# Kernel tuning notes

Hardware: AMD Instinct MI355X
Metric: run time of the kernel (lower is better)

## Reference

```python
import jax, jax.numpy as jnp
import numpy as np

EMBED = 2048
HEADS = 32
HEAD_DIM = EMBED // HEADS
ALPHA = 12.0
MAX_SEQ = 1024
GAMMA = -ALPHA / MAX_SEQ  # clipped softmax lower stretch
ETA = 1.0


def setup_inputs() -> dict:
    key = jax.random.key(0)
    ks = jax.random.split(key, 12)
    B, T, E, H, D = 4, 1024, EMBED, HEADS, HEAD_DIM
    s = 1.0 / np.sqrt(E)
    hidden_states = jax.random.normal(ks[0], (B, T, E), dtype=jnp.float32)
    # causal attention mask: True = attend
    causal = jnp.tril(jnp.ones((T, T), dtype=bool))
    attention_mask = jnp.broadcast_to(causal[None, None], (B, 1, T, T))
    Wq = jax.random.normal(ks[1], (E, E), dtype=jnp.float32) * s
    bq = jnp.zeros((E,), dtype=jnp.float32)
    Wk = jax.random.normal(ks[2], (E, E), dtype=jnp.float32) * s
    bk = jnp.zeros((E,), dtype=jnp.float32)
    Wv = jax.random.normal(ks[3], (E, E), dtype=jnp.float32) * s
    bv = jnp.zeros((E,), dtype=jnp.float32)
    Wo = jax.random.normal(ks[4], (E, E), dtype=jnp.float32) * s
    bo = jnp.zeros((E,), dtype=jnp.float32)
    gate_w = jax.random.normal(ks[5], (H, D), dtype=jnp.float32) * (1.0 / np.sqrt(D))
    gate_b = jnp.zeros((H,), dtype=jnp.float32)
    return {"hidden_states": hidden_states, "attention_mask": attention_mask,
            "Wq": Wq, "bq": bq, "Wk": Wk, "bk": bk, "Wv": Wv, "bv": bv,
            "Wo": Wo, "bo": bo, "gate_w": gate_w, "gate_b": gate_b}


def clipped_softmax(x, gamma, eta):
    p = jax.nn.softmax(x, axis=-1)
    return jnp.clip((eta - gamma) * p + gamma, 0.0, 1.0)


def reference(hidden_states, attention_mask, Wq, bq, Wk, bk, Wv, bv, Wo, bo, gate_w, gate_b):
    B, T, E = hidden_states.shape
    H, D = HEADS, HEAD_DIM
    scaling = D ** -0.5
    neg_min = jnp.finfo(hidden_states.dtype).min

    q = ((hidden_states @ Wq.T + bq) * scaling).reshape(B, T, H, D)
    k = (hidden_states @ Wk.T + bk).reshape(B, T, H, D)
    v = (hidden_states @ Wv.T + bv).reshape(B, T, H, D)

    # scores: [B,H,T,S]
    scores = jnp.einsum('bthd,bshd->bhts', q, k)
    mask_add = jnp.where(attention_mask, 0.0, neg_min)  # [B,1,T,S]
    scores = jnp.maximum(scores + mask_add, neg_min)

    probs = clipped_softmax(scores, GAMMA, ETA)

    attn_out = jnp.einsum('bhts,bshd->bhtd', probs, v)  # [B,H,T,D]

    # conditional_per_token gate: per-head Linear(head_dim -> 1), sigmoid
    x_heads = hidden_states.reshape(B, T, H, D)
    gate = jax.nn.sigmoid(jnp.einsum('bthd,hd->bht', x_heads, gate_w) + gate_b[None, :, None])
    attn_out = attn_out * gate[..., None]  # gate_scaling_factor = 1.0

    out = attn_out.transpose(0, 2, 1, 3).reshape(B, T, E)
    return out @ Wo.T + bo
```

## Files before the change

### kernel.cpp

```cpp
#include <hip/hip_runtime.h>
#include <hip/hip_bf16.h>

typedef unsigned short ushort_t;
using short8 = __attribute__((ext_vector_type(8))) short;
using f32x4  = __attribute__((ext_vector_type(4))) float;

constexpr int B_ = 4;
constexpr int T_ = 1024;
constexpr int E_ = 2048;
constexpr int H_ = 32;
constexpr int D_ = 64;
constexpr float GAMMA_  = -12.0f / 1024.0f;
constexpr float ONE_MG_ = 1.0f - GAMMA_;

__device__ __forceinline__ ushort_t f2bf(float f) {
  union { float f; unsigned int i; } x; x.f = f;
  unsigned int u = x.i;
  u += 0x7fffu + ((u >> 16) & 1u);
  return (ushort_t)(u >> 16);
}

__global__ __launch_bounds__(256) void f2bf_multi(
    const float* __restrict__ x,
    const float* __restrict__ Wq, const float* __restrict__ Wk,
    const float* __restrict__ Wv, const float* __restrict__ Wo,
    ushort_t* __restrict__ xb,
    ushort_t* __restrict__ wqb, ushort_t* __restrict__ wkb,
    ushort_t* __restrict__ wvb, ushort_t* __restrict__ wob) {
  const int i = blockIdx.x * 256 + threadIdx.x;
  const float* src; ushort_t* dst; int off;
  if (i < 2097152)      { src = x;  dst = xb;  off = i; }
  else if (i < 3145728) { src = Wq; dst = wqb; off = i - 2097152; }
  else if (i < 4194304) { src = Wk; dst = wkb; off = i - 3145728; }
  else if (i < 5242880) { src = Wv; dst = wvb; off = i - 4194304; }
  else                  { src = Wo; dst = wob; off = i - 5242880; }
  const float4 f = ((const float4*)src)[off];
  ushort4 u; u.x = f2bf(f.x); u.y = f2bf(f.y); u.z = f2bf(f.z); u.w = f2bf(f.w);
  ((ushort4*)dst)[off] = u;
}

__device__ __forceinline__ void gl_lds16(const ushort_t* g, ushort_t* l) {
  __builtin_amdgcn_global_load_lds(
      (const __attribute__((address_space(1))) void*)g,
      (__attribute__((address_space(3))) void*)l, 16, 0, 0);
}

__global__ __launch_bounds__(256) void gemm_qkv(
    const ushort_t* __restrict__ xb,
    const ushort_t* __restrict__ wq, const ushort_t* __restrict__ wk,
    const ushort_t* __restrict__ wv,
    const float* __restrict__ bq, const float* __restrict__ bk,
    const float* __restrict__ bv,
    ushort_t* __restrict__ qout, ushort_t* __restrict__ kout,
    ushort_t* __restrict__ vtout) {
  constexpr int K = 2048;
  __shared__ ushort_t As[128 * 32];
  __shared__ ushort_t Bs[128 * 32];
  const int which = blockIdx.x >> 4;
  const int colt  = blockIdx.x & 15;
  const ushort_t* Wt  = (which == 0) ? wq : (which == 1) ? wk : wv;
  const float*   bias = (which == 0) ? bq : (which == 1) ? bk : bv;
  const float    scale = (which == 0) ? 0.125f : 1.0f;

  const int tid = threadIdx.x;
  const int wave = tid >> 6, lane = tid & 63;
  const int lane15 = lane & 15, quad = lane >> 4;
  const int row0 = blockIdx.y * 128, col0 = colt * 128;
  const int srow = lane >> 2;
  const int scol = (lane & 3) * 8;
  const ushort_t* Ag0 = xb + (size_t)(row0 + wave * 32 + srow) * K + scol;
  const ushort_t* Ag1 = Ag0 + 16 * (size_t)K;
  const ushort_t* Bg0 = Wt + (size_t)(col0 + wave * 32 + srow) * K + scol;
  const ushort_t* Bg1 = Bg0 + 16 * (size_t)K;
  ushort_t* Al0 = &As[(wave * 32     ) * 32];
  ushort_t* Al1 = &As[(wave * 32 + 16) * 32];
  ushort_t* Bl0 = &Bs[(wave * 32     ) * 32];
  ushort_t* Bl1 = &Bs[(wave * 32 + 16) * 32];
  const int wr = wave >> 1, wc = wave & 1;
  const int q8 = quad * 8;

  f32x4 acc[4][4];
#pragma unroll
  for (int i = 0; i < 4; i++)
#pragma unroll
    for (int j = 0; j < 4; j++) acc[i][j] = (f32x4){0.f, 0.f, 0.f, 0.f};

  for (int k0 = 0; k0 < K; k0 += 32) {
    __syncthreads();
    gl_lds16(Ag0 + k0, Al0);
    gl_lds16(Ag1 + k0, Al1);
    gl_lds16(Bg0 + k0, Bl0);
    gl_lds16(Bg1 + k0, Bl1);
    __syncthreads();
    short8 a_f[4], b_f[4];
#pragma unroll
    for (int i = 0; i < 4; i++)
      a_f[i] = *(const short8*)&As[(wr * 64 + i * 16 + lane15) * 32 + q8];
#pragma unroll
    for (int j = 0; j < 4; j++)
      b_f[j] = *(const short8*)&Bs[(wc * 64 + j * 16 + lane15) * 32 + q8];
#pragma unroll
    for (int i = 0; i < 4; i++)
#pragma unroll
      for (int j = 0; j < 4; j++)
        acc[i][j] = __builtin_amdgcn_mfma_f32_16x16x32_bf16(
            a_f[i], b_f[j], acc[i][j], 0, 0, 0);
  }

  ushort_t* outp = (which == 0) ? qout : (which == 1) ? kout : vtout;
#pragma unroll
  for (int j = 0; j < 4; j++) {
    const int c = col0 + wc * 64 + j * 16 + lane15;
    const float bia = bias[c];
#pragma unroll
    for (int i = 0; i < 4; i++) {
#pragma unroll
      for (int reg = 0; reg < 4; reg++) {
        const int r = row0 + wr * 64 + i * 16 + quad * 4 + reg;
        const float val = (acc[i][j][reg] + bia) * scale;
        const int b = r >> 10, t = r & 1023, h = c >> 6, d = c & 63;
        if (which < 2)
          outp[(((size_t)(b * 32 + h)) * 1024 + t) * 64 + d] = f2bf(val);
        else
          outp[(((size_t)(b * 32 + h)) * 64 + d) * 1024 + t] = f2bf(val);
      }
    }
  }
}

__global__ __launch_bounds__(256) void gemm_out(
    const ushort_t* __restrict__ A, const ushort_t* __restrict__ Wt,
    const float* __restrict__ bias, float* __restrict__ Cout) {
  constexpr int K = 2048;
  __shared__ ushort_t As[128 * 32];
  __shared__ ushort_t Bs[128 * 32];
  const int tid = threadIdx.x;
  const int wave = tid >> 6, lane = tid & 63;
  const int lane15 = lane & 15, quad = lane >> 4;
  const int row0 = blockIdx.y * 128, col0 = blockIdx.x * 128;
  const int srow = lane >> 2;
  const int scol = (lane & 3) * 8;
  const ushort_t* Ag0 = A  + (size_t)(row0 + wave * 32 + srow) * K + scol;
  const ushort_t* Ag1 = Ag0 + 16 * (size_t)K;
  const ushort_t* Bg0 = Wt + (size_t)(col0 + wave * 32 + srow) * K + scol;
  const ushort_t* Bg1 = Bg0 + 16 * (size_t)K;
  ushort_t* Al0 = &As[(wave * 32     ) * 32];
  ushort_t* Al1 = &As[(wave * 32 + 16) * 32];
  ushort_t* Bl0 = &Bs[(wave * 32     ) * 32];
  ushort_t* Bl1 = &Bs[(wave * 32 + 16) * 32];
  const int wr = wave >> 1, wc = wave & 1;
  const int q8 = quad * 8;

  f32x4 acc[4][4];
#pragma unroll
  for (int i = 0; i < 4; i++)
#pragma unroll
    for (int j = 0; j < 4; j++) acc[i][j] = (f32x4){0.f, 0.f, 0.f, 0.f};

  for (int k0 = 0; k0 < K; k0 += 32) {
    __syncthreads();
    gl_lds16(Ag0 + k0, Al0);
    gl_lds16(Ag1 + k0, Al1);
    gl_lds16(Bg0 + k0, Bl0);
    gl_lds16(Bg1 + k0, Bl1);
    __syncthreads();
    short8 a_f[4], b_f[4];
#pragma unroll
    for (int i = 0; i < 4; i++)
      a_f[i] = *(const short8*)&As[(wr * 64 + i * 16 + lane15) * 32 + q8];
#pragma unroll
    for (int j = 0; j < 4; j++)
      b_f[j] = *(const short8*)&Bs[(wc * 64 + j * 16 + lane15) * 32 + q8];
#pragma unroll
    for (int i = 0; i < 4; i++)
#pragma unroll
      for (int j = 0; j < 4; j++)
        acc[i][j] = __builtin_amdgcn_mfma_f32_16x16x32_bf16(
            a_f[i], b_f[j], acc[i][j], 0, 0, 0);
  }

#pragma unroll
  for (int j = 0; j < 4; j++) {
    const int c = col0 + wc * 64 + j * 16 + lane15;
    const float bia = bias[c];
#pragma unroll
    for (int i = 0; i < 4; i++) {
#pragma unroll
      for (int reg = 0; reg < 4; reg++) {
        const int r = row0 + wr * 64 + i * 16 + quad * 4 + reg;
        Cout[(size_t)r * 2048 + c] = acc[i][j][reg] + bia;
      }
    }
  }
}

__global__ __launch_bounds__(256) void gates_kernel(
    const float* __restrict__ x, const float* __restrict__ gw,
    const float* __restrict__ gb, float* __restrict__ gates) {
  const int idx = blockIdx.x * 256 + threadIdx.x;
  const int h = idx & 31;
  const int bt = idx >> 5;
  const float* xp = x + (size_t)bt * E_ + h * D_;
  const float* wp = gw + h * D_;
  float s = 0.f;
#pragma unroll
  for (int d = 0; d < D_; d += 4) {
    const float4 xv = *(const float4*)&xp[d];
    const float4 wv = *(const float4*)&wp[d];
    s = fmaf(xv.x, wv.x, s); s = fmaf(xv.y, wv.y, s);
    s = fmaf(xv.z, wv.z, s); s = fmaf(xv.w, wv.w, s);
  }
  s += gb[h];
  gates[idx] = 1.0f / (1.0f + __expf(-s));
}

__global__ __launch_bounds__(256) void attn_mfma(
    const ushort_t* __restrict__ q, const ushort_t* __restrict__ k,
    const ushort_t* __restrict__ vt, const float* __restrict__ gates,
    ushort_t* __restrict__ attn_out) {
  __shared__ ushort_t Pb[4][16 * 72];

  const int tid = threadIdx.x;
  const int wave = tid >> 6, lane = tid & 63;
  const int l15 = lane & 15, quad = lane >> 4;
  const int bx = blockIdx.x;
  const int xcd = bx & 7, w = bx >> 3;
  const int bh = xcd * 16 + (w & 15);
  const int qt = 7 - (w >> 4);
  const int h = bh & 31, b = bh >> 5;
  const int t0 = qt * 128;
  const ushort_t* qbase = q  + (size_t)bh * (T_ * D_);
  const ushort_t* kbase = k  + (size_t)bh * (T_ * D_);
  const ushort_t* vbase = vt + (size_t)bh * (D_ * T_);

  short8 qf[2][2];
#pragma unroll
  for (int s = 0; s < 2; s++) {
    const ushort_t* qp =
        qbase + (size_t)(t0 + s * 64 + wave * 16 + l15) * 64 + quad * 8;
    qf[s][0] = *(const short8*)qp;
    qf[s][1] = *(const short8*)(qp + 32);
  }

  const int nkt = 2 * qt + 2;
  const int rb0 = qt * 8 + wave;
  const int rb1 = qt * 8 + 4 + wave;

  float l_part[2][4] = {};

  for (int kt = 0; kt < nkt; kt++) {
    f32x4 sc[2][4];
#pragma unroll
    for (int j = 0; j < 4; j++) {
      const int cb = kt * 4 + j;
      if (cb > rb1) {
        sc[0][j] = sc[1][j] = (f32x4){-3.0e38f, -3.0e38f, -3.0e38f, -3.0e38f};
        continue;
      }
      const ushort_t* kp =
          kbase + (size_t)(kt * 64 + j * 16 + l15) * 64 + quad * 8;
      const short8 kf0 = *(const short8*)kp;
      const short8 kf1 = *(const short8*)(kp + 32);
#pragma unroll
      for (int s = 0; s < 2; s++) {
        const int rb = s ? rb1 : rb0;
        if (cb > rb) {
          sc[s][j] = (f32x4){-3.0e38f, -3.0e38f, -3.0e38f, -3.0e38f};
          continue;
        }
        f32x4 z = (f32x4){0.f, 0.f, 0.f, 0.f};
        z = __builtin_amdgcn_mfma_f32_16x16x32_bf16(qf[s][0], kf0, z, 0, 0, 0);
        z = __builtin_amdgcn_mfma_f32_16x16x32_bf16(qf[s][1], kf1, z, 0, 0, 0);
        if (cb == rb) {
#pragma unroll
          for (int r = 0; r < 4; r++)
            if (l15 > quad * 4 + r) z[r] = -3.0e38f;
        }
        sc[s][j] = z;
      }
    }
#pragma unroll
    for (int s = 0; s < 2; s++) {
      if (kt * 4 > (s ? rb1 : rb0)) continue;
#pragma unroll
      for (int r = 0; r < 4; r++)
        l_part[s][r] += __expf(sc[s][0][r]) + __expf(sc[s][1][r]) +
                        __expf(sc[s][2][r]) + __expf(sc[s][3][r]);
    }
  }

  float c1[2][4];
#pragma unroll
  for (int s = 0; s < 2; s++)
#pragma unroll
    for (int r = 0; r < 4; r++) {
      float e = l_part[s][r];
      e += __shfl_xor(e, 1); e += __shfl_xor(e, 2);
      e += __shfl_xor(e, 4); e += __shfl_xor(e, 8);
      c1[s][r] = ONE_MG_ / e;
    }

  f32x4 acc[2][4];
#pragma unroll
  for (int s = 0; s < 2; s++)
#pragma unroll
    for (int jd = 0; jd < 4; jd++) acc[s][jd] = (f32x4){0.f, 0.f, 0.f, 0.f};

  for (int kt = 0; kt < nkt; kt++) {
    f32x4 sc[2][4];
#pragma unroll
    for (int j = 0; j < 4; j++) {
      const int cb = kt * 4 + j;
      if (cb > rb1) {
        sc[0][j] = sc[1][j] = (f32x4){-3.0e38f, -3.0e38f, -3.0e38f, -3.0e38f};
        continue;
      }
      const ushort_t* kp =
          kbase + (size_t)(kt * 64 + j * 16 + l15) * 64 + quad * 8;
      const short8 kf0 = *(const short8*)kp;
      const short8 kf1 = *(const short8*)(kp + 32);
#pragma unroll
      for (int s = 0; s < 2; s++) {
        const int rb = s ? rb1 : rb0;
        if (cb > rb) {
          sc[s][j] = (f32x4){-3.0e38f, -3.0e38f, -3.0e38f, -3.0e38f};
          continue;
        }
        f32x4 z = (f32x4){0.f, 0.f, 0.f, 0.f};
        z = __builtin_amdgcn_mfma_f32_16x16x32_bf16(qf[s][0], kf0, z, 0, 0, 0);
        z = __builtin_amdgcn_mfma_f32_16x16x32_bf16(qf[s][1], kf1, z, 0, 0, 0);
        if (cb == rb) {
#pragma unroll
          for (int r = 0; r < 4; r++)
            if (l15 > quad * 4 + r) z[r] = -3.0e38f;
        }
        sc[s][j] = z;
      }
    }
    short8 pf[2][2];
#pragma unroll
    for (int s = 0; s < 2; s++) {
      if (kt * 4 > (s ? rb1 : rb0)) continue;
      ushort_t* pb = &Pb[wave][0];
#pragma unroll
      for (int j = 0; j < 4; j++) {
#pragma unroll
        for (int r = 0; r < 4; r++) {
          float p = fmaf(c1[s][r], __expf(sc[s][j][r]), GAMMA_);
          p = fminf(fmaxf(p, 0.f), 1.f);
          pb[(quad * 4 + r) * 72 + j * 16 + l15] = f2bf(p);
        }
      }
      pf[s][0] = *(const short8*)&pb[l15 * 72 + quad * 8];
      pf[s][1] = *(const short8*)&pb[l15 * 72 + 32 + quad * 8];
    }
    const bool do0 = (kt * 4 <= rb0);
#pragma unroll
    for (int jd = 0; jd < 4; jd++) {
      const ushort_t* vp =
          vbase + (size_t)(jd * 16 + l15) * 1024 + kt * 64 + quad * 8;
      const short8 vf0 = *(const short8*)vp;
      const short8 vf1 = *(const short8*)(vp + 32);
      if (do0) {
        acc[0][jd] =
            __builtin_amdgcn_mfma_f32_16x16x32_bf16(pf[0][0], vf0, acc[0][jd], 0, 0, 0);
        acc[0][jd] =
            __builtin_amdgcn_mfma_f32_16x16x32_bf16(pf[0][1], vf1, acc[0][jd], 0, 0, 0);
      }
      acc[1][jd] =
          __builtin_amdgcn_mfma_f32_16x16x32_bf16(pf[1][0], vf0, acc[1][jd], 0, 0, 0);
      acc[1][jd] =
          __builtin_amdgcn_mfma_f32_16x16x32_bf16(pf[1][1], vf1, acc[1][jd], 0, 0, 0);
    }
  }

#pragma unroll
  for (int s = 0; s < 2; s++) {
#pragma unroll
    for (int r = 0; r < 4; r++) {
      const int t = t0 + s * 64 + wave * 16 + quad * 4 + r;
      const float g = gates[((size_t)b * T_ + t) * H_ + h];
      ushort_t* op = attn_out + ((size_t)b * T_ + t) * E_ + h * 64;
#pragma unroll
      for (int jd = 0; jd < 4; jd++)
        op[jd * 16 + l15] = f2bf(acc[s][jd][r] * g);
    }
  }
}

extern "C" void kernel_launch(void* const* d_in, const int* in_sizes, int n_in,
                              void* d_out, int out_size, void* d_ws, size_t ws_size,
                              hipStream_t stream) {
  (void)in_sizes; (void)n_in; (void)out_size; (void)ws_size;
  const float* x  = (const float*)d_in[0];
  const float* Wq = (const float*)d_in[2];
  const float* bq = (const float*)d_in[3];
  const float* Wk = (const float*)d_in[4];
  const float* bk = (const float*)d_in[5];
  const float* Wv = (const float*)d_in[6];
  const float* bv = (const float*)d_in[7];
  const float* Wo = (const float*)d_in[8];
  const float* bo = (const float*)d_in[9];
  const float* gw = (const float*)d_in[10];
  const float* gb = (const float*)d_in[11];
  float* out = (float*)d_out;

  char* W = (char*)d_ws;
  ushort_t* xb  = (ushort_t*)(W + 0);
  ushort_t* wqb = (ushort_t*)(W + 16777216);
  ushort_t* wkb = (ushort_t*)(W + 25165824);
  ushort_t* wvb = (ushort_t*)(W + 33554432);
  ushort_t* wob = (ushort_t*)(W + 41943040);
  ushort_t* qb  = (ushort_t*)(W + 50331648);
  ushort_t* kb  = (ushort_t*)(W + 67108864);
  ushort_t* vtb = (ushort_t*)(W + 83886080);
  ushort_t* ab  = (ushort_t*)(W + 100663296);
  float*    gts = (float*)(W + 117440512);

  f2bf_multi<<<24576, 256, 0, stream>>>(x, Wq, Wk, Wv, Wo,
                                        xb, wqb, wkb, wvb, wob);

  gemm_qkv<<<dim3(48, 32), 256, 0, stream>>>(xb, wqb, wkb, wvb,
                                             bq, bk, bv, qb, kb, vtb);
  gates_kernel<<<512, 256, 0, stream>>>(x, gw, gb, gts);
  attn_mfma<<<1024, 256, 0, stream>>>(qb, kb, vtb, gts, ab);
  gemm_out<<<dim3(16, 32), 256, 0, stream>>>(ab, wob, bo, out);
}
```

Measured before the change: 467.9 us.

## Stage K tiles through double-buffered shared memory in attention kernel

New measurement: 434.0 us. 1.08x faster.

```diff
diff --git a/kernel.cpp b/kernel.cpp
--- a/kernel.cpp
+++ b/kernel.cpp
@@ -218,17 +218,18 @@
     const ushort_t* __restrict__ q, const ushort_t* __restrict__ k,
     const ushort_t* __restrict__ vt, const float* __restrict__ gates,
     ushort_t* __restrict__ attn_out) {
+  __shared__ ushort_t Kt[2][64 * 72];
   __shared__ ushort_t Pb[4][16 * 72];
 
   const int tid = threadIdx.x;
   const int wave = tid >> 6, lane = tid & 63;
   const int l15 = lane & 15, quad = lane >> 4;
   const int bx = blockIdx.x;
-  const int xcd = bx & 7, w = bx >> 3;
-  const int bh = xcd * 16 + (w & 15);
-  const int qt = 7 - (w >> 4);
+  const int qt = 7 - (bx >> 7);
+  const int bh = bx & 127;
   const int h = bh & 31, b = bh >> 5;
   const int t0 = qt * 128;
+  const int qt8 = qt * 8;
   const ushort_t* qbase = q  + (size_t)bh * (T_ * D_);
   const ushort_t* kbase = k  + (size_t)bh * (T_ * D_);
   const ushort_t* vbase = vt + (size_t)bh * (D_ * T_);
@@ -242,13 +243,31 @@
     qf[s][1] = *(const short8*)(qp + 32);
   }
 
+  const int srow = tid >> 2;
+  const int scol = (tid & 3) * 16;
   const int nkt = 2 * qt + 2;
-  const int rb0 = qt * 8 + wave;
-  const int rb1 = qt * 8 + 4 + wave;
+  const int rb0 = qt8 + wave;
+  const int rb1 = qt8 + 4 + wave;
 
   float l_part[2][4] = {};
 
+  {
+    const ushort_t* kg = &kbase[(size_t)srow * 64 + scol];
+    const short8 k0 = *(const short8*)kg;
+    const short8 k1 = *(const short8*)(kg + 8);
+    ushort_t* kl = &Kt[0][srow * 72 + scol];
+    *(short8*)kl = k0; *(short8*)(kl + 8) = k1;
+  }
+  __syncthreads();
   for (int kt = 0; kt < nkt; kt++) {
+    const int buf = kt & 1;
+    const bool more = (kt + 1 < nkt);
+    short8 nk0, nk1;
+    if (more) {
+      const ushort_t* kg = &kbase[(size_t)((kt + 1) * 64 + srow) * 64 + scol];
+      nk0 = *(const short8*)kg;
+      nk1 = *(const short8*)(kg + 8);
+    }
     f32x4 sc[2][4];
 #pragma unroll
     for (int j = 0; j < 4; j++) {
@@ -257,8 +276,7 @@
         sc[0][j] = sc[1][j] = (f32x4){-3.0e38f, -3.0e38f, -3.0e38f, -3.0e38f};
         continue;
       }
-      const ushort_t* kp =
-          kbase + (size_t)(kt * 64 + j * 16 + l15) * 64 + quad * 8;
+      const ushort_t* kp = &Kt[buf][(j * 16 + l15) * 72 + quad * 8];
       const short8 kf0 = *(const short8*)kp;
       const short8 kf1 = *(const short8*)(kp + 32);
 #pragma unroll
@@ -287,6 +305,11 @@
         l_part[s][r] += __expf(sc[s][0][r]) + __expf(sc[s][1][r]) +
                         __expf(sc[s][2][r]) + __expf(sc[s][3][r]);
     }
+    if (more) {
+      ushort_t* kl = &Kt[buf ^ 1][srow * 72 + scol];
+      *(short8*)kl = nk0; *(short8*)(kl + 8) = nk1;
+      __syncthreads();
+    }
   }
 
   float c1[2][4];
@@ -306,7 +329,24 @@
 #pragma unroll
     for (int jd = 0; jd < 4; jd++) acc[s][jd] = (f32x4){0.f, 0.f, 0.f, 0.f};
 
+  __syncthreads();
+  {
+    const ushort_t* kg = &kbase[(size_t)srow * 64 + scol];
+    const short8 k0 = *(const short8*)kg;
+    const short8 k1 = *(const short8*)(kg + 8);
+    ushort_t* kl = &Kt[0][srow * 72 + scol];
+    *(short8*)kl = k0; *(short8*)(kl + 8) = k1;
+  }
+  __syncthreads();
   for (int kt = 0; kt < nkt; kt++) {
+    const int buf = kt & 1;
+    const bool more = (kt + 1 < nkt);
+    short8 nk0, nk1;
+    if (more) {
+      const ushort_t* kg = &kbase[(size_t)((kt + 1) * 64 + srow) * 64 + scol];
+      nk0 = *(const short8*)kg;
+      nk1 = *(const short8*)(kg + 8);
+    }
     f32x4 sc[2][4];
 #pragma unroll
     for (int j = 0; j < 4; j++) {
@@ -315,8 +355,7 @@
         sc[0][j] = sc[1][j] = (f32x4){-3.0e38f, -3.0e38f, -3.0e38f, -3.0e38f};
         continue;
       }
-      const ushort_t* kp =
-          kbase + (size_t)(kt * 64 + j * 16 + l15) * 64 + quad * 8;
+      const ushort_t* kp = &Kt[buf][(j * 16 + l15) * 72 + quad * 8];
       const short8 kf0 = *(const short8*)kp;
       const short8 kf1 = *(const short8*)(kp + 32);
 #pragma unroll
@@ -337,10 +376,11 @@
         sc[s][j] = z;
       }
     }
+    const bool do0 = (kt * 4 <= rb0);
     short8 pf[2][2];
 #pragma unroll
     for (int s = 0; s < 2; s++) {
-      if (kt * 4 > (s ? rb1 : rb0)) continue;
+      if (s == 0 && !do0) continue;
       ushort_t* pb = &Pb[wave][0];
 #pragma unroll
       for (int j = 0; j < 4; j++) {
@@ -354,7 +394,6 @@
       pf[s][0] = *(const short8*)&pb[l15 * 72 + quad * 8];
       pf[s][1] = *(const short8*)&pb[l15 * 72 + 32 + quad * 8];
     }
-    const bool do0 = (kt * 4 <= rb0);
 #pragma unroll
     for (int jd = 0; jd < 4; jd++) {
       const ushort_t* vp =
@@ -371,6 +410,11 @@
           __builtin_amdgcn_mfma_f32_16x16x32_bf16(pf[1][0], vf0, acc[1][jd], 0, 0, 0);
       acc[1][jd] =
           __builtin_amdgcn_mfma_f32_16x16x32_bf16(pf[1][1], vf1, acc[1][jd], 0, 0, 0);
+    }
+    if (more) {
+      ushort_t* kl = &Kt[buf ^ 1][srow * 72 + scol];
+      *(short8*)kl = nk0; *(short8*)(kl + 8) = nk1;
+      __syncthreads();
     }
   }
 
```
